# Kernel tuning notes

Measured on AMD Instinct MI355X. Metric: run time of the kernel, lower is better.

## Reference

```python
import jax, jax.numpy as jnp
import numpy as np

Q = 10        # icosahedral diamonds
M = 128       # 2**dggrid_level
L = Q * M * M # 163840 icosahedral points
KS = 9        # kernel_size / knn neighbors


def setup_inputs() -> dict:
    key = jax.random.key(0)
    k1, k2, k3, k4 = jax.random.split(key, 4)
    b, c, h, w = 1, 128, 256, 512
    x = jax.random.normal(k1, (b, c, h, w), dtype=jnp.float32)
    codeskmin = jax.random.randint(k2, (L, KS), 0, h * w, dtype=jnp.int32)
    att_w = jax.random.normal(k3, (KS, 2, KS), dtype=jnp.float32) * 0.1
    att_b = jnp.zeros((KS,), dtype=jnp.float32)
    depth_w = jax.random.normal(k4, (c, KS), dtype=jnp.float32) * 0.1
    depth_b = jnp.zeros((c,), dtype=jnp.float32)
    gamma = jnp.ones((c,), dtype=jnp.float32)
    beta = jnp.zeros((c,), dtype=jnp.float32)
    return {"x": x, "codeskmin": codeskmin, "att_w": att_w, "att_b": att_b,
            "depth_w": depth_w, "depth_b": depth_b, "gamma": gamma, "beta": beta}


def reference(x, codeskmin, att_w, att_b, depth_w, depth_b, gamma, beta):
    b, c, h, w = x.shape
    xf = x.reshape(b, c, h * w)
    # KNN gather: (b, c, L, KS)
    xe = xf[:, :, codeskmin]
    # --- SpatialAttentionModule_v1 ---
    avg = jnp.mean(xe, axis=1)           # (b, L, KS)
    mx = jnp.max(xe, axis=1)             # (b, L, KS)
    feat = jnp.stack([avg, mx], axis=1)  # (b, 2, L, KS)
    # Conv2d(2 -> KS, kernel (1,KS), no pad): reduces neighbor axis fully
    att = jnp.einsum('bilk,oik->bol', feat, att_w) + att_b[None, :, None]  # (b, KS, L)
    att = jax.nn.sigmoid(att)
    att = att.transpose(0, 2, 1)[:, None, :, :]  # (b, 1, L, KS)
    xe = att * xe + xe
    # --- depthwise conv over neighbor axis ---
    out = jnp.einsum('bclk,ck->bcl', xe, depth_w) + depth_b[None, :, None]  # (b, c, L)
    # rearrange 'b c (q h w) -> (b q) c h w'
    out = out.reshape(b, c, Q, M, M).transpose(0, 2, 1, 3, 4).reshape(b * Q, c, M, M)
    # BatchNorm (training-mode batch stats)
    mean = jnp.mean(out, axis=(0, 2, 3), keepdims=True)
    var = jnp.var(out, axis=(0, 2, 3), keepdims=True)
    out = (out - mean) * jax.lax.rsqrt(var + 1e-5)
    out = out * gamma[None, :, None, None] + beta[None, :, None, None]
    # Swish
    out = out * jax.nn.sigmoid(out)
    return out
```

## Files before the change

### kernel.cpp

```cpp
#include <hip/hip_runtime.h>
#include <hip/hip_bf16.h>

#define HW 131072
#define NCH 128
#define KS 9
#define L_TOTAL 163840
#define LPW 16

static __device__ __forceinline__ float bflo(unsigned int p) { return __uint_as_float(p << 16); }
static __device__ __forceinline__ float bfhi(unsigned int p) { return __uint_as_float(p & 0xffff0000u); }
static __device__ __forceinline__ unsigned short f2bf(float f) {
    unsigned int x = __float_as_uint(f);
    return (unsigned short)((x + 0x7fffu + ((x >> 16) & 1u)) >> 16);
}
static __device__ __forceinline__ unsigned int pack2(float a, float b) {
    return (unsigned int)f2bf(a) | ((unsigned int)f2bf(b) << 16);
}

__global__ __launch_bounds__(256) void transpose_x_kernel(
    const float2* __restrict__ xf,
    unsigned int* __restrict__ xT,
    float2* __restrict__ meanmaxP)
{
    __shared__ unsigned short tile[128][130];
    __shared__ float ps[4][128];
    __shared__ float pm[4][128];
    const int tid = threadIdx.x;
    const int lane = tid & 63;
    const int wave = tid >> 6;
    const int p0 = blockIdx.x * 128;

    float s0 = 0.f, s1 = 0.f;
    float m0 = -3.4e38f, m1 = -3.4e38f;
    #pragma unroll 8
    for (int it = 0; it < 32; ++it) {
        int c = wave + (it << 2);
        float2 v = xf[(long)c * (HW / 2) + (p0 >> 1) + lane];
        *reinterpret_cast<unsigned int*>(&tile[c][lane * 2]) = pack2(v.x, v.y);
        s0 += v.x; s1 += v.y;
        m0 = fmaxf(m0, v.x); m1 = fmaxf(m1, v.y);
    }
    ps[wave][2 * lane] = s0; ps[wave][2 * lane + 1] = s1;
    pm[wave][2 * lane] = m0; pm[wave][2 * lane + 1] = m1;
    __syncthreads();

    #pragma unroll 8
    for (int it = 0; it < 32; ++it) {
        int p = wave + (it << 2);
        unsigned short a = tile[2 * lane][p];
        unsigned short b = tile[2 * lane + 1][p];
        xT[(long)(p0 + p) * 64 + lane] = (unsigned int)a | ((unsigned int)b << 16);
    }
    if (tid < 128) {
        float s = ps[0][tid] + ps[1][tid] + ps[2][tid] + ps[3][tid];
        float m = fmaxf(fmaxf(pm[0][tid], pm[1][tid]), fmaxf(pm[2][tid], pm[3][tid]));
        meanmaxP[p0 + tid] = make_float2(s * 0.0078125f, m);
    }
}

__global__ __launch_bounds__(256) void encoder_main_kernel(
    const unsigned int* __restrict__ xT,
    const float2* __restrict__ meanmaxP,
    const int* __restrict__ cks,
    const float* __restrict__ att_w,
    const float* __restrict__ att_b,
    const float* __restrict__ depth_w,
    const float* __restrict__ depth_b,
    float* __restrict__ out,
    float* __restrict__ gsum, float* __restrict__ gsq)
{
    __shared__ __align__(16) char smem[38400];
    float* attw = (float*)smem;
    float* attb = (float*)(smem + 648);
    int*   lcks = (int*)(smem + 688);
    float* mult = (float*)(smem + 2992);
    float* tile = (float*)(smem + 5312);
    float* red  = (float*)smem;

    const int tid = threadIdx.x;
    const int lane = tid & 63;
    const int wave = tid >> 6;
    const int c0 = lane * 2, c1 = c0 + 1;
    const int base_l = blockIdx.x * 64;

    if (tid < 162) attw[tid] = att_w[tid];
    if (tid < KS) attb[tid] = att_b[tid];
    for (int j = tid; j < 64 * KS; j += 256) lcks[j] = cks[base_l * KS + j];

    float dw0[KS], dw1[KS];
    #pragma unroll
    for (int k = 0; k < KS; ++k) {
        dw0[k] = depth_w[c0 * KS + k];
        dw1[k] = depth_w[c1 * KS + k];
    }
    const float db0 = depth_b[c0], db1 = depth_b[c1];
    __syncthreads();

    {
        const int l_local = tid >> 2;
        const int sub = tid & 3;
        if (sub < 3) {
            float mean[KS], mx[KS];
            #pragma unroll
            for (int k = 0; k < KS; ++k) {
                float2 mm = meanmaxP[lcks[l_local * KS + k]];
                mean[k] = mm.x; mx[k] = mm.y;
            }
            #pragma unroll
            for (int oo = 0; oo < 3; ++oo) {
                int o = sub * 3 + oo;
                float logit = attb[o];
                #pragma unroll
                for (int k = 0; k < KS; ++k) {
                    logit = fmaf(mean[k], attw[o * 18 + k], logit);
                    logit = fmaf(mx[k],   attw[o * 18 + 9 + k], logit);
                }
                mult[l_local * KS + o] = 1.0f + 1.0f / (1.0f + __expf(-logit));
            }
        }
    }
    __syncthreads();

    float sum0 = 0.f, sum1 = 0.f, sq0 = 0.f, sq1 = 0.f;

    for (int li = 0; li < LPW; ++li) {
        const int l_local = wave * LPW + li;
        float acc0 = db0, acc1 = db1;
        #pragma unroll
        for (int k = 0; k < KS; ++k) {
            int idx = __builtin_amdgcn_readfirstlane(lcks[l_local * KS + k]);
            unsigned int p = xT[(long)idx * 64 + lane];
            float mk = mult[l_local * KS + k];
            acc0 = fmaf(bflo(p) * mk, dw0[k], acc0);
            acc1 = fmaf(bfhi(p) * mk, dw1[k], acc1);
        }
        tile[l_local * 129 + c0] = acc0;
        tile[l_local * 129 + c1] = acc1;
        sum0 += acc0; sum1 += acc1;
        sq0 = fmaf(acc0, acc0, sq0);
        sq1 = fmaf(acc1, acc1, sq1);
    }

    __syncthreads();
    red[0 * 256 + tid] = sum0;
    red[1 * 256 + tid] = sum1;
    red[2 * 256 + tid] = sq0;
    red[3 * 256 + tid] = sq1;
    __syncthreads();

    const int q = base_l >> 14;
    const int r0 = base_l & 16383;
    #pragma unroll 8
    for (int it = 0; it < 32; ++it) {
        int c = wave + (it << 2);
        out[((long)(q * NCH + c) << 14) + r0 + lane] = tile[lane * 129 + c];
    }

    const int g = tid >> 6;
    const int i = tid & 63;
    float t = red[g * 256 + i] + red[g * 256 + 64 + i] +
              red[g * 256 + 128 + i] + red[g * 256 + 192 + i];
    float* dst = (g & 2) ? gsq : gsum;
    atomicAdd(&dst[2 * i + (g & 1)], t);
}

__global__ __launch_bounds__(256) void finalize_kernel(
    float4* __restrict__ out,
    const float* __restrict__ gsum, const float* __restrict__ gsq,
    const float* __restrict__ gamma, const float* __restrict__ beta)
{
    const long i4 = (long)blockIdx.x * 256 + threadIdx.x;
    const int c = (int)(i4 >> 12) & 127;

    const float invN = 1.0f / (float)L_TOTAL;
    const float m = gsum[c] * invN;
    const float var = gsq[c] * invN - m * m;
    const float sc = gamma[c] * rsqrtf(var + 1e-5f);
    const float sh = beta[c] - m * sc;

    float4 v = out[i4];
    float z0 = fmaf(v.x, sc, sh);
    float z1 = fmaf(v.y, sc, sh);
    float z2 = fmaf(v.z, sc, sh);
    float z3 = fmaf(v.w, sc, sh);
    v.x = z0 / (1.0f + __expf(-z0));
    v.y = z1 / (1.0f + __expf(-z1));
    v.z = z2 / (1.0f + __expf(-z2));
    v.w = z3 / (1.0f + __expf(-z3));
    out[i4] = v;
}

extern "C" void kernel_launch(void* const* d_in, const int* in_sizes, int n_in,
                              void* d_out, int out_size, void* d_ws, size_t ws_size,
                              hipStream_t stream) {
    const float2* x_f2 = (const float2*)d_in[0];
    const int* cks     = (const int*)d_in[1];
    const float* aw    = (const float*)d_in[2];
    const float* ab    = (const float*)d_in[3];
    const float* dw    = (const float*)d_in[4];
    const float* db    = (const float*)d_in[5];
    const float* gm    = (const float*)d_in[6];
    const float* bt    = (const float*)d_in[7];
    float* out         = (float*)d_out;

    char* ws = (char*)d_ws;
    unsigned int* xT  = (unsigned int*)ws;
    float2* meanmaxP  = (float2*)(ws + 33554432);
    float* gsum       = (float*)(ws + 33554432 + 1048576);
    float* gsq        = gsum + NCH;

    hipMemsetAsync(gsum, 0, 2 * NCH * sizeof(float), stream);

    transpose_x_kernel<<<HW / 128, 256, 0, stream>>>(x_f2, xT, meanmaxP);
    encoder_main_kernel<<<L_TOTAL / 64, 256, 0, stream>>>(
        xT, meanmaxP, cks, aw, ab, dw, db, out, gsum, gsq);
    finalize_kernel<<<out_size / 4 / 256, 256, 0, stream>>>(
        (float4*)out, gsum, gsq, gm, bt);
}
```

Before: 320.9 us.

## Prefetch next point's gathered rows and swizzle transpose LDS tile

The main kernel now software-pipelines the KNN gather: the nine bf16 rows for the next output point are loaded into registers while the current point is accumulated, and the loop is fully unrolled. This is meant to hide global gather latency within each wave. Launch bounds add a minimum-occupancy hint of 4, which may force register spills given the doubled prefetch registers. The transpose kernel replaces the padded LDS tile with an XOR-free rotated swizzle, writing 16-bit elements and reading packed 32-bit pairs, to cut bank conflicts and drop the pack step.

```diff
diff --git a/kernel.cpp b/kernel.cpp
--- a/kernel.cpp
+++ b/kernel.cpp
@@ -13,22 +13,20 @@
     unsigned int x = __float_as_uint(f);
     return (unsigned short)((x + 0x7fffu + ((x >> 16) & 1u)) >> 16);
 }
-static __device__ __forceinline__ unsigned int pack2(float a, float b) {
-    return (unsigned int)f2bf(a) | ((unsigned int)f2bf(b) << 16);
-}
 
 __global__ __launch_bounds__(256) void transpose_x_kernel(
     const float2* __restrict__ xf,
     unsigned int* __restrict__ xT,
     float2* __restrict__ meanmaxP)
 {
-    __shared__ unsigned short tile[128][130];
+    __shared__ unsigned short tile[128 * 128];
     __shared__ float ps[4][128];
     __shared__ float pm[4][128];
     const int tid = threadIdx.x;
     const int lane = tid & 63;
     const int wave = tid >> 6;
     const int p0 = blockIdx.x * 128;
+    const int pa = 2 * lane, pb = 2 * lane + 1;
 
     float s0 = 0.f, s1 = 0.f;
     float m0 = -3.4e38f, m1 = -3.4e38f;
@@ -36,20 +34,21 @@
     for (int it = 0; it < 32; ++it) {
         int c = wave + (it << 2);
         float2 v = xf[(long)c * (HW / 2) + (p0 >> 1) + lane];
-        *reinterpret_cast<unsigned int*>(&tile[c][lane * 2]) = pack2(v.x, v.y);
+        tile[pa * 128 + ((c + 2 * pa) & 127)] = f2bf(v.x);
+        tile[pb * 128 + ((c + 2 * pb) & 127)] = f2bf(v.y);
         s0 += v.x; s1 += v.y;
         m0 = fmaxf(m0, v.x); m1 = fmaxf(m1, v.y);
     }
-    ps[wave][2 * lane] = s0; ps[wave][2 * lane + 1] = s1;
-    pm[wave][2 * lane] = m0; pm[wave][2 * lane + 1] = m1;
+    ps[wave][pa] = s0; ps[wave][pb] = s1;
+    pm[wave][pa] = m0; pm[wave][pb] = m1;
     __syncthreads();
 
     #pragma unroll 8
     for (int it = 0; it < 32; ++it) {
         int p = wave + (it << 2);
-        unsigned short a = tile[2 * lane][p];
-        unsigned short b = tile[2 * lane + 1][p];
-        xT[(long)(p0 + p) * 64 + lane] = (unsigned int)a | ((unsigned int)b << 16);
+        int colr = (2 * lane + 2 * p) & 127;
+        unsigned int d = *reinterpret_cast<const unsigned int*>(&tile[p * 128 + colr]);
+        xT[(long)(p0 + p) * 64 + lane] = d;
     }
     if (tid < 128) {
         float s = ps[0][tid] + ps[1][tid] + ps[2][tid] + ps[3][tid];
@@ -58,7 +57,7 @@
     }
 }
 
-__global__ __launch_bounds__(256) void encoder_main_kernel(
+__global__ __launch_bounds__(256, 4) void encoder_main_kernel(
     const unsigned int* __restrict__ xT,
     const float2* __restrict__ meanmaxP,
     const int* __restrict__ cks,
@@ -122,23 +121,39 @@
     __syncthreads();
 
     float sum0 = 0.f, sum1 = 0.f, sq0 = 0.f, sq1 = 0.f;
-
+    const int l0 = wave * LPW;
+
+    unsigned int pv[KS], pn[KS];
+    #pragma unroll
+    for (int k = 0; k < KS; ++k) {
+        int idx = __builtin_amdgcn_readfirstlane(lcks[l0 * KS + k]);
+        pv[k] = xT[(long)idx * 64 + lane];
+    }
+
+    #pragma unroll
     for (int li = 0; li < LPW; ++li) {
-        const int l_local = wave * LPW + li;
+        const int l_local = l0 + li;
+        if (li + 1 < LPW) {
+            #pragma unroll
+            for (int k = 0; k < KS; ++k) {
+                int idx = __builtin_amdgcn_readfirstlane(lcks[(l_local + 1) * KS + k]);
+                pn[k] = xT[(long)idx * 64 + lane];
+            }
+        }
         float acc0 = db0, acc1 = db1;
         #pragma unroll
         for (int k = 0; k < KS; ++k) {
-            int idx = __builtin_amdgcn_readfirstlane(lcks[l_local * KS + k]);
-            unsigned int p = xT[(long)idx * 64 + lane];
             float mk = mult[l_local * KS + k];
-            acc0 = fmaf(bflo(p) * mk, dw0[k], acc0);
-            acc1 = fmaf(bfhi(p) * mk, dw1[k], acc1);
+            acc0 = fmaf(bflo(pv[k]) * mk, dw0[k], acc0);
+            acc1 = fmaf(bfhi(pv[k]) * mk, dw1[k], acc1);
         }
         tile[l_local * 129 + c0] = acc0;
         tile[l_local * 129 + c1] = acc1;
         sum0 += acc0; sum1 += acc1;
         sq0 = fmaf(acc0, acc0, sq0);
         sq1 = fmaf(acc1, acc1, sq1);
+        #pragma unroll
+        for (int k = 0; k < KS; ++k) pv[k] = pn[k];
     }
 
     __syncthreads();
```

Measured after the change: 320.0 us. Within noise of the previous version (-0.3%).
